# Kernel tuning notes

Measured on AMD Instinct MI355X. Metric: run time of the kernel, lower is better.

## Reference

```python
import jax, jax.numpy as jnp
import numpy as np
from jax import lax

EPS = 1e-6

def _instance_norm(x):
    # torch: std over flattened spatial, unbiased (ddof=1), + 1e-6
    b, c = x.shape[:2]
    xf = x.reshape(b, c, -1)
    mean = xf.mean(axis=2)[:, :, None, None]
    std = (jnp.std(xf, axis=2, ddof=1) + EPS)[:, :, None, None]
    return (x - mean) / std

def _conv1x1(x, w, b):
    # w: [O, I], x: [B, I, H, W]
    return jnp.einsum('oi,bihw->bohw', w, x) + b[None, :, None, None]

def _adaattn(content, style, ckey, skey, fw, fb, gw, gb, hw, hb):
    F = _conv1x1(ckey, fw, fb)   # [b, Ck, hc, wc]
    G = _conv1x1(skey, gw, gb)   # [b, Ck, hs, ws]
    H = _conv1x1(style, hw, hb)  # [b, Cv, hs, ws]
    b_, Ck, hc, wc = F.shape
    hs, ws = G.shape[2], G.shape[3]
    Fq = F.reshape(b_, Ck, hc * wc).transpose(0, 2, 1)   # [b, Nc, Ck]
    Gk = G.reshape(b_, Ck, hs * ws)                      # [b, Ck, Ns]
    Vs = H.reshape(b_, -1, hs * ws).transpose(0, 2, 1)   # [b, Ns, Cv]
    # Ns == hs*ws <= max_sample (4096) for these shapes -> no subsampling branch
    S = jax.nn.softmax(jnp.einsum('bnc,bcm->bnm', Fq, Gk), axis=-1)  # [b, Nc, Ns]
    mean = jnp.einsum('bnm,bmv->bnv', S, Vs)              # attention-weighted mean
    ex2 = jnp.einsum('bnm,bmv->bnv', S, Vs * Vs)          # E[x^2]
    std = jnp.sqrt(jax.nn.relu(ex2 - mean * mean))        # sqrt(relu(E[x^2]-E[x]^2))
    mean = mean.reshape(b_, hc, wc, -1).transpose(0, 3, 1, 2)
    std = std.reshape(b_, hc, wc, -1).transpose(0, 3, 1, 2)
    return std * _instance_norm(content) + mean

def _upsample2(x):
    return jnp.repeat(jnp.repeat(x, 2, axis=2), 2, axis=3)

def _conv3x3_reflect(x, w, b):
    xp = jnp.pad(x, ((0, 0), (0, 0), (1, 1), (1, 1)), mode='reflect')
    y = lax.conv_general_dilated(xp, w, window_strides=(1, 1), padding='VALID',
                                 dimension_numbers=('NCHW', 'OIHW', 'NCHW'))
    return y + b[None, :, None, None]


def setup_inputs() -> dict:
    key = jax.random.key(0)
    ks = jax.random.split(key, 16)
    f32 = jnp.float32
    d = {}
    d['content4_1'] = jax.random.normal(ks[0], (1, 512, 128, 128), f32)
    d['style4_1'] = jax.random.normal(ks[1], (1, 512, 64, 64), f32)
    d['content5_1'] = jax.random.normal(ks[2], (1, 512, 64, 64), f32)
    d['style5_1'] = jax.random.normal(ks[3], (1, 512, 32, 32), f32)
    d['content4_1_key'] = jax.random.normal(ks[4], (1, 960, 128, 128), f32)
    d['style4_1_key'] = jax.random.normal(ks[5], (1, 960, 64, 64), f32)
    d['content5_1_key'] = jax.random.normal(ks[6], (1, 1472, 64, 64), f32)
    d['style5_1_key'] = jax.random.normal(ks[7], (1, 1472, 32, 32), f32)
    def w2(k, o, i):
        return jax.random.normal(k, (o, i), f32) / np.sqrt(i).astype(np.float32)
    d['f4_w'] = w2(ks[8], 960, 960); d['f4_b'] = jnp.zeros((960,), f32)
    d['g4_w'] = w2(ks[9], 960, 960); d['g4_b'] = jnp.zeros((960,), f32)
    d['h4_w'] = w2(ks[10], 512, 512); d['h4_b'] = jnp.zeros((512,), f32)
    d['f5_w'] = w2(ks[11], 1472, 1472); d['f5_b'] = jnp.zeros((1472,), f32)
    d['g5_w'] = w2(ks[12], 1472, 1472); d['g5_b'] = jnp.zeros((1472,), f32)
    d['h5_w'] = w2(ks[13], 512, 512); d['h5_b'] = jnp.zeros((512,), f32)
    d['conv_w'] = jax.random.normal(ks[14], (512, 512, 3, 3), f32) / np.sqrt(512 * 9).astype(np.float32)
    d['conv_b'] = jnp.zeros((512,), f32)
    return d


def reference(content4_1, style4_1, content5_1, style5_1,
              content4_1_key, style4_1_key, content5_1_key, style5_1_key,
              f4_w, f4_b, g4_w, g4_b, h4_w, h4_b,
              f5_w, f5_b, g5_w, g5_b, h5_w, h5_b,
              conv_w, conv_b):
    a4 = _adaattn(content4_1, style4_1, content4_1_key, style4_1_key,
                  f4_w, f4_b, g4_w, g4_b, h4_w, h4_b)
    a5 = _adaattn(content5_1, style5_1, content5_1_key, style5_1_key,
                  f5_w, f5_b, g5_w, g5_b, h5_w, h5_b)
    return _conv3x3_reflect(a4 + _upsample2(a5), conv_w, conv_b)
```

## Files before the change

kernel.cpp:

```cpp
#include <hip/hip_runtime.h>
#include <math.h>


typedef _Float16 half8 __attribute__((ext_vector_type(8)));
typedef float f32x4 __attribute__((ext_vector_type(4)));

__device__ __forceinline__ void async16(const void* g, void* lds) {
    __builtin_amdgcn_global_load_lds(
        (const __attribute__((address_space(1))) void*)g,
        (__attribute__((address_space(3))) void*)lds, 16, 0, 0);
}

__device__ inline float wave_sum64(float v) {
#pragma unroll
    for (int o = 32; o > 0; o >>= 1) v += __shfl_xor(v, o, 64);
    return v;
}

template <int OUT>
__global__ __launch_bounds__(256, 2) void mgemm_hl(
    const _Float16* __restrict__ Ahi, const _Float16* __restrict__ Alo,
    const _Float16* __restrict__ Bhi, const _Float16* __restrict__ Blo,
    float* __restrict__ Cf, _Float16* __restrict__ Chi,
    _Float16* __restrict__ Clo, int K, int lda, int ldb, int ldc) {
    __shared__ _Float16 Ash[4096], Asl[4096], Bsh[4096], Bsl[4096];
    const int t = threadIdx.x, wave = t >> 6, lane = t & 63;
    const int bm = blockIdx.y * 128, bn = blockIdx.x * 128;
    const int wr = (wave >> 1) * 64, wc = (wave & 1) * 64;
    const int lq = lane >> 4, lr = lane & 15;
    const int srow = wave * 32 + (lane >> 2);
    const int scolg = (lane & 3) ^ ((lane >> 3) & 3);

    f32x4 acc[4][4] = {};

    const size_t aoff = (size_t)(bm + srow) * lda * 2 + scolg * 16;
    const size_t boff = (size_t)(bn + srow) * ldb * 2 + scolg * 16;
    const char* pAh = (const char*)Ahi + aoff;
    const char* pAl = (const char*)Alo + aoff;
    const char* pBh = (const char*)Bhi + boff;
    const char* pBl = (const char*)Blo + boff;
    const size_t ar = (size_t)16 * lda * 2, br = (size_t)16 * ldb * 2;
    _Float16* dAh = Ash + wave * 1024;
    _Float16* dAl = Asl + wave * 1024;
    _Float16* dBh = Bsh + wave * 1024;
    _Float16* dBl = Bsl + wave * 1024;
    const int key = (lr >> 1) & 3;

    for (int k0 = 0; k0 < K; k0 += 32) {
        __syncthreads();
        async16(pAh, dAh);
        async16(pAh + ar, dAh + 512);
        async16(pAl, dAl);
        async16(pAl + ar, dAl + 512);
        async16(pBh, dBh);
        async16(pBh + br, dBh + 512);
        async16(pBl, dBl);
        async16(pBl + br, dBl + 512);
        pAh += 64;
        pAl += 64;
        pBh += 64;
        pBl += 64;
        __syncthreads();

        half8 ah[4], al[4], bh[4], bl[4];
#pragma unroll
        for (int i = 0; i < 4; i++) {
            const int ro = (wr + i * 16 + lr) * 32 + ((lq ^ key) * 8);
            ah[i] = *(const half8*)&Ash[ro];
            al[i] = *(const half8*)&Asl[ro];
        }
#pragma unroll
        for (int j = 0; j < 4; j++) {
            const int ro = (wc + j * 16 + lr) * 32 + ((lq ^ key) * 8);
            bh[j] = *(const half8*)&Bsh[ro];
            bl[j] = *(const half8*)&Bsl[ro];
        }
#pragma unroll
        for (int i = 0; i < 4; i++)
#pragma unroll
            for (int j = 0; j < 4; j++) {
                acc[i][j] = __builtin_amdgcn_mfma_f32_16x16x32_f16(
                    ah[i], bl[j], acc[i][j], 0, 0, 0);
                acc[i][j] = __builtin_amdgcn_mfma_f32_16x16x32_f16(
                    al[i], bh[j], acc[i][j], 0, 0, 0);
                acc[i][j] = __builtin_amdgcn_mfma_f32_16x16x32_f16(
                    ah[i], bh[j], acc[i][j], 0, 0, 0);
            }
    }
#pragma unroll
    for (int i = 0; i < 4; i++) {
        const int m0 = bm + wr + i * 16 + lq * 4;
#pragma unroll
        for (int j = 0; j < 4; j++) {
            const int n = bn + wc + j * 16 + lr;
#pragma unroll
            for (int r = 0; r < 4; r++) {
                const float v = acc[i][j][r];
                const size_t o = (size_t)(m0 + r) * ldc + n;
                if (OUT == 0) {
                    Cf[o] = v;
                } else {
                    _Float16 h = (_Float16)v;
                    Chi[o] = h;
                    Clo[o] = (_Float16)(v - (float)h);
                }
            }
        }
    }
}

template <int BIAS_MODE, int OUT_MODE, bool CONV>
__global__ __launch_bounds__(256, 2) void mgemm16(
    const _Float16* __restrict__ A, const _Float16* __restrict__ B,
    const float* __restrict__ bias, float* __restrict__ Cf,
    _Float16* __restrict__ Ch, int K, int lda, int ldb, int ldc,
    size_t splitStride) {
    __shared__ _Float16 As[128 * 32];
    __shared__ _Float16 Bs[128 * 32];
    const int t = threadIdx.x, wave = t >> 6, lane = t & 63;
    const int bm = blockIdx.y * 128, bn = blockIdx.x * 128;
    const int kbase = blockIdx.z * K;
    const int wr = (wave >> 1) * 64, wc = (wave & 1) * 64;
    const int lq = lane >> 4, lr = lane & 15;
    const int srow = wave * 32 + (lane >> 2);
    const int scolg = (lane & 3) ^ ((lane >> 3) & 3);

    f32x4 acc[4][4] = {};

    const char* Ap = (const char*)A +
                     ((size_t)(bm + srow) * lda + kbase) * 2 + scolg * 16;
    const char* Bp = (const char*)B +
                     ((size_t)(bn + srow) * ldb + kbase) * 2 + scolg * 16;
    const size_t Astep = (size_t)16 * lda * 2;
    const size_t Bstep = (size_t)16 * ldb * 2;
    _Float16* As0 = &As[(wave * 32) * 32];
    _Float16* As1 = &As[(wave * 32 + 16) * 32];
    _Float16* Bs0 = &Bs[(wave * 32) * 32];
    _Float16* Bs1 = &Bs[(wave * 32 + 16) * 32];
    const int key = (lr >> 1) & 3;

    for (int k0 = 0; k0 < K; k0 += 32) {
        __syncthreads();
        async16(Ap, As0);
        async16(Ap + Astep, As1);
        if (CONV) {
            const int kg = kbase + k0;
            const int rI = kg >> 9;
            const int dy = rI / 3, dx = rI - 3 * dy;
            const int ci0 = kg & 511;
            const char* Bc =
                (const char*)B +
                (((size_t)(blockIdx.x + dy) * 130 + srow + dx) * 512 + ci0) * 2 +
                scolg * 16;
            async16(Bc, Bs0);
            async16(Bc + (size_t)16 * 512 * 2, Bs1);
        } else {
            async16(Bp, Bs0);
            async16(Bp + Bstep, Bs1);
            Bp += 64;
        }
        Ap += 64;
        __syncthreads();

        half8 af[4], bf[4];
#pragma unroll
        for (int i = 0; i < 4; i++)
            af[i] = *(const half8*)&As[(wr + i * 16 + lr) * 32 + (lq ^ key) * 8];
#pragma unroll
        for (int j = 0; j < 4; j++)
            bf[j] = *(const half8*)&Bs[(wc + j * 16 + lr) * 32 + (lq ^ key) * 8];
#pragma unroll
        for (int i = 0; i < 4; i++)
#pragma unroll
            for (int j = 0; j < 4; j++)
                acc[i][j] = __builtin_amdgcn_mfma_f32_16x16x32_f16(
                    af[i], bf[j], acc[i][j], 0, 0, 0);
    }

    float* Co = (OUT_MODE == 0) ? Cf + (size_t)blockIdx.z * splitStride : nullptr;
#pragma unroll
    for (int i = 0; i < 4; i++) {
        const int m0 = bm + wr + i * 16 + lq * 4;
#pragma unroll
        for (int j = 0; j < 4; j++) {
            const int n = bn + wc + j * 16 + lr;
#pragma unroll
            for (int r = 0; r < 4; r++) {
                const int m = m0 + r;
                float v = acc[i][j][r];
                if (BIAS_MODE == 2) v += bias[m];
                if (OUT_MODE == 0) {
                    Co[(size_t)m * ldc + n] = v;
                } else {
                    Ch[(size_t)m * ldc + n] = (_Float16)v;
                    Ch[(size_t)(m + 512) * ldc + n] = (_Float16)(v * v);
                }
            }
        }
    }
}

__global__ __launch_bounds__(256) void transpose_hilo(
    const float* __restrict__ src, _Float16* __restrict__ dsthi,
    _Float16* __restrict__ dstlo, long srcld, int dstld, int nvalid,
    int cvalid) {
    __shared__ float tile[32][33];
    const int t = threadIdx.x, tx = t & 31, ty = t >> 5;
    const int n0 = blockIdx.x * 32, c0 = blockIdx.y * 32;
    const int n = n0 + tx;
#pragma unroll
    for (int i = 0; i < 4; i++) {
        int c = c0 + ty + i * 8;
        tile[ty + i * 8][tx] =
            (c < cvalid && n < nvalid) ? src[(size_t)c * srcld + n] : 0.f;
    }
    __syncthreads();
#pragma unroll
    for (int i = 0; i < 4; i++) {
        int nn = ty + i * 8;
        float v = tile[tx][nn];
        _Float16 h = (_Float16)v;
        size_t o = (size_t)(n0 + nn) * dstld + c0 + tx;
        dsthi[o] = h;
        dstlo[o] = (_Float16)(v - (float)h);
    }
}

__global__ __launch_bounds__(256) void transpose_cvt16(
    const float* __restrict__ src, _Float16* __restrict__ dst, long srcld,
    int dstld) {
    __shared__ float tile[32][33];
    const int t = threadIdx.x, tx = t & 31, ty = t >> 5;
    const int n0 = blockIdx.x * 32, c0 = blockIdx.y * 32;
#pragma unroll
    for (int i = 0; i < 4; i++)
        tile[ty + i * 8][tx] = src[(size_t)(c0 + ty + i * 8) * srcld + n0 + tx];
    __syncthreads();
#pragma unroll
    for (int i = 0; i < 4; i++) {
        int nn = ty + i * 8;
        dst[(size_t)(n0 + nn) * dstld + c0 + tx] = (_Float16)tile[tx][nn];
    }
}

__global__ __launch_bounds__(256) void cvt16(const float* __restrict__ src,
                                             _Float16* __restrict__ dst) {
    int i = blockIdx.x * 256 + threadIdx.x;
    dst[i] = (_Float16)src[i];
}

__global__ __launch_bounds__(256) void convw_perm(const float* __restrict__ src,
                                                  _Float16* __restrict__ dst) {
    int idx = blockIdx.x * 256 + threadIdx.x;
    int o = idx / 4608, rem = idx - o * 4608;
    int r = rem >> 9, ci = rem & 511;
    dst[idx] = (_Float16)src[(size_t)o * 4608 + ci * 9 + r];
}

__global__ __launch_bounds__(256) void fold_vec(
    const float* __restrict__ mat, const float* __restrict__ vec,
    const float* __restrict__ addc, float* __restrict__ outv, int C, int Nout,
    long ldm) {
    __shared__ float red[4][64];
    const int t = threadIdx.x, lane = t & 63, seg = t >> 6;
    const int n = blockIdx.x * 64 + lane;
    const int chunk = (C + 3) >> 2;
    const int start = seg * chunk;
    const int end = min(C, start + chunk);
    float s0 = 0.f, s1 = 0.f, s2 = 0.f, s3 = 0.f;
    if (n < Nout) {
        int c = start;
        for (; c + 3 < end; c += 4) {
            s0 = fmaf(vec[c], mat[(size_t)c * ldm + n], s0);
            s1 = fmaf(vec[c + 1], mat[(size_t)(c + 1) * ldm + n], s1);
            s2 = fmaf(vec[c + 2], mat[(size_t)(c + 2) * ldm + n], s2);
            s3 = fmaf(vec[c + 3], mat[(size_t)(c + 3) * ldm + n], s3);
        }
        for (; c < end; c++) s0 = fmaf(vec[c], mat[(size_t)c * ldm + n], s0);
    }
    red[seg][lane] = (s0 + s1) + (s2 + s3);
    __syncthreads();
    if (seg == 0 && n < Nout)
        outv[n] = red[0][lane] + red[1][lane] + red[2][lane] + red[3][lane] +
                  (addc ? addc[0] : 0.f);
}

__global__ __launch_bounds__(256) void dotbb(const float* __restrict__ a,
                                             const float* __restrict__ b,
                                             float* __restrict__ out, int C) {
    __shared__ float red[4];
    const int t = threadIdx.x;
    float s = 0.f;
    for (int c = t; c < C; c += 256) s = fmaf(a[c], b[c], s);
    s = wave_sum64(s);
    if ((t & 63) == 0) red[t >> 6] = s;
    __syncthreads();
    if (t == 0) out[0] = red[0] + red[1] + red[2] + red[3];
}

__global__ __launch_bounds__(256) void softmax_f16(
    const float* __restrict__ L, const float* __restrict__ rr,
    _Float16* __restrict__ S, int cols) {
    __shared__ float red_m[4], red_s[4];
    const int t = threadIdx.x;
    const float* p = L + (size_t)blockIdx.x * cols;
    _Float16* q = S + (size_t)blockIdx.x * cols;
    float mt = -3.0e38f, st = 0.f;
    for (int c = t; c < cols; c += 256) {
        float v = p[c] + rr[c];
        if (v > mt) {
            st = st * __expf(mt - v) + 1.f;
            mt = v;
        } else {
            st += __expf(v - mt);
        }
    }
#pragma unroll
    for (int o = 32; o > 0; o >>= 1) {
        float m2 = __shfl_xor(mt, o, 64), s2 = __shfl_xor(st, o, 64);
        float m = fmaxf(mt, m2);
        st = st * __expf(mt - m) + s2 * __expf(m2 - m);
        mt = m;
    }
    if ((t & 63) == 0) {
        red_m[t >> 6] = mt;
        red_s[t >> 6] = st;
    }
    __syncthreads();
    float M = fmaxf(fmaxf(red_m[0], red_m[1]), fmaxf(red_m[2], red_m[3]));
    float Ssum = red_s[0] * __expf(red_m[0] - M) +
                 red_s[1] * __expf(red_m[1] - M) +
                 red_s[2] * __expf(red_m[2] - M) +
                 red_s[3] * __expf(red_m[3] - M);
    float inv = 1.f / Ssum;
    for (int c = t; c < cols; c += 256)
        q[c] = (_Float16)(__expf(p[c] + rr[c] - M) * inv);
}

__global__ __launch_bounds__(256) void chanstats_kernel(
    const float* __restrict__ x, float* __restrict__ cm,
    float* __restrict__ cstd, int N) {
    __shared__ float rs[4], rs2[4];
    const int t = threadIdx.x;
    const float* p = x + (size_t)blockIdx.x * N;
    float s = 0.f, s2 = 0.f;
    for (int i = t; i < N; i += 256) {
        float v = p[i];
        s += v;
        s2 = fmaf(v, v, s2);
    }
    s = wave_sum64(s);
    s2 = wave_sum64(s2);
    if ((t & 63) == 0) {
        rs[t >> 6] = s;
        rs2[t >> 6] = s2;
    }
    __syncthreads();
    if (t == 0) {
        float S = rs[0] + rs[1] + rs[2] + rs[3];
        float S2 = rs2[0] + rs2[1] + rs2[2] + rs2[3];
        float mean = S / N;
        float var = fmaxf((S2 - S * mean) / (N - 1), 0.f);
        cm[blockIdx.x] = mean;
        cstd[blockIdx.x] = sqrtf(var) + 1e-6f;
    }
}

__global__ __launch_bounds__(256) void epilogue5(
    const float* __restrict__ pv, const float* __restrict__ content,
    const float* __restrict__ cm, const float* __restrict__ cstd,
    _Float16* __restrict__ a5t) {
    int idx = blockIdx.x * 256 + threadIdx.x;
    int n = idx >> 9, c = idx & 511;
    float mean = pv[(size_t)n * 1024 + c];
    float ex2 = pv[(size_t)n * 1024 + 512 + c];
    float sd = sqrtf(fmaxf(ex2 - mean * mean, 0.f));
    float cn = (content[(size_t)c * 4096 + n] - cm[c]) / cstd[c];
    a5t[idx] = (_Float16)(fmaf(sd, cn, mean));
}

__global__ __launch_bounds__(256) void epilogue4(
    const float* __restrict__ part, const float* __restrict__ content,
    const float* __restrict__ cm, const float* __restrict__ cstd,
    const _Float16* __restrict__ a5t, _Float16* __restrict__ pad4t, int n0) {
    int idx = blockIdx.x * 256 + threadIdx.x;
    int r = idx >> 9, c = idx & 511;
    int n = n0 + r;
    const size_t SS = (size_t)1024 * 1024;
    float mean = 0.f, ex2 = 0.f;
#pragma unroll
    for (int z = 0; z < 4; z++) {
        mean += part[z * SS + (size_t)r * 1024 + c];
        ex2 += part[z * SS + (size_t)r * 1024 + 512 + c];
    }
    float sd = sqrtf(fmaxf(ex2 - mean * mean, 0.f));
    float cn = (content[(size_t)c * 16384 + n] - cm[c]) / cstd[c];
    int y = n >> 7, x = n & 127;
    float up = (float)a5t[(size_t)((y >> 1) * 64 + (x >> 1)) * 512 + c];
    pad4t[(size_t)((y + 1) * 130 + (x + 1)) * 512 + c] =
        (_Float16)(fmaf(sd, cn, mean) + up);
}

__global__ __launch_bounds__(256) void border_kernel(_Float16* __restrict__ pad) {
    int idx = blockIdx.x * 256 + threadIdx.x;
    int pos = idx >> 9, c = idx & 511;
    int py, px;
    if (pos < 130) { py = 0; px = pos; }
    else if (pos < 260) { py = 129; px = pos - 130; }
    else if (pos < 388) { py = pos - 260 + 1; px = 0; }
    else { py = pos - 388 + 1; px = 129; }
    int sy = py == 0 ? 2 : (py == 129 ? 127 : py);
    int sx = px == 0 ? 2 : (px == 129 ? 127 : px);
    pad[(size_t)(py * 130 + px) * 512 + c] =
        pad[(size_t)(sy * 130 + sx) * 512 + c];
}


extern "C" void kernel_launch(void* const* d_in, const int* in_sizes, int n_in,
                              void* d_out, int out_size, void* d_ws,
                              size_t ws_size, hipStream_t stream) {
    (void)in_sizes; (void)n_in; (void)out_size; (void)ws_size;
    const float* content4 = (const float*)d_in[0];
    const float* style4 = (const float*)d_in[1];
    const float* content5 = (const float*)d_in[2];
    const float* style5 = (const float*)d_in[3];
    const float* ckey4 = (const float*)d_in[4];
    const float* skey4 = (const float*)d_in[5];
    const float* ckey5 = (const float*)d_in[6];
    const float* skey5 = (const float*)d_in[7];
    const float* f4w = (const float*)d_in[8];
    const float* f4b = (const float*)d_in[9];
    const float* g4w = (const float*)d_in[10];
    const float* g4b = (const float*)d_in[11];
    const float* h4w = (const float*)d_in[12];
    const float* h4b = (const float*)d_in[13];
    const float* f5w = (const float*)d_in[14];
    const float* f5b = (const float*)d_in[15];
    const float* g5w = (const float*)d_in[16];
    const float* g5b = (const float*)d_in[17];
    const float* h5w = (const float*)d_in[18];
    const float* h5b = (const float*)d_in[19];
    const float* convw = (const float*)d_in[20];
    const float* convb = (const float*)d_in[21];
    float* out = (float*)d_out;
    char* ws = (char*)d_ws;

    _Float16* PAD4T = (_Float16*)(ws + 0);
    _Float16* A5T = (_Float16*)(ws + 17305600);
    float* STATS = (float*)(ws + 21499904);
    _Float16* H4W = (_Float16*)(ws + 21508096);
    _Float16* H5W = (_Float16*)(ws + 22032384);
    _Float16* CONVW = (_Float16*)(ws + 22556672);
    float* U5 = (float*)(ws + 27275264);
    float* R5 = (float*)(ws + 27283456);
    float* U4 = (float*)(ws + 27291648);
    float* R4 = (float*)(ws + 27299840);
    float* BB5 = (float*)(ws + 27316224);
    float* BB4 = (float*)(ws + 27316480);
    char* A0 = ws + 27320320;

    float* cm4 = STATS, *cstd4 = STATS + 512, *cm5 = STATS + 1024,
         *cstd5 = STATS + 1536;

    chanstats_kernel<<<512, 256, 0, stream>>>(content5, cm5, cstd5, 4096);
    chanstats_kernel<<<512, 256, 0, stream>>>(content4, cm4, cstd4, 16384);
    cvt16<<<1024, 256, 0, stream>>>(h4w, H4W);
    cvt16<<<1024, 256, 0, stream>>>(h5w, H5W);
    convw_perm<<<9216, 256, 0, stream>>>(convw, CONVW);

    {
        _Float16* M5h = (_Float16*)(A0 + 0);
        _Float16* M5l = (_Float16*)(A0 + 4718592);
        _Float16* FWh = (_Float16*)(A0 + 9437184);
        _Float16* FWl = (_Float16*)(A0 + 14155776);
        _Float16* GWh = (_Float16*)(A0 + 18874368);
        _Float16* GWl = (_Float16*)(A0 + 23592960);
        _Float16* SKh = (_Float16*)(A0 + 9437184);
        _Float16* SKl = (_Float16*)(A0 + 12582912);
        _Float16* T5h = (_Float16*)(A0 + 15728640);
        _Float16* T5l = (_Float16*)(A0 + 18874368);
        _Float16* STT5 = (_Float16*)(A0 + 0);
        _Float16* HCAT5 = (_Float16*)(A0 + 1048576);
        _Float16* CKh = (_Float16*)(A0 + 22020096);
        _Float16* CKl = (_Float16*)(A0 + 34603008);
        float* LOG5 = (float*)(A0 + 47185920);
        _Float16* S5 = (_Float16*)(A0 + 63963136);

        dotbb<<<1, 256, 0, stream>>>(f5b, g5b, BB5, 1472);
        fold_vec<<<23, 256, 0, stream>>>(g5w, f5b, nullptr, U5, 1472, 1472, 1472);
        fold_vec<<<16, 256, 0, stream>>>(skey5, U5, BB5, R5, 1472, 1024, 1024);

        transpose_hilo<<<dim3(48, 48), 256, 0, stream>>>(f5w, FWh, FWl, 1472,
                                                         1536, 1472, 1472);
        transpose_hilo<<<dim3(48, 48), 256, 0, stream>>>(g5w, GWh, GWl, 1472,
                                                         1536, 1472, 1472);
        mgemm_hl<1><<<dim3(12, 12), 256, 0, stream>>>(
            FWh, FWl, GWh, GWl, nullptr, M5h, M5l, 1536, 1536, 1536, 1536);
        transpose_hilo<<<dim3(32, 48), 256, 0, stream>>>(skey5, SKh, SKl, 1024,
                                                         1536, 1024, 1472);
        mgemm_hl<1><<<dim3(12, 8), 256, 0, stream>>>(
            SKh, SKl, M5h, M5l, nullptr, T5h, T5l, 1536, 1536, 1536, 1536);
        transpose_cvt16<<<dim3(32, 16), 256, 0, stream>>>(style5, STT5, 1024, 512);
        mgemm16<2, 2, false><<<dim3(8, 4), 256, 0, stream>>>(
            H5W, STT5, h5b, nullptr, HCAT5, 512, 512, 512, 1024, 0);
        transpose_hilo<<<dim3(128, 48), 256, 0, stream>>>(ckey5, CKh, CKl, 4096,
                                                          1536, 4096, 1472);
        mgemm_hl<0><<<dim3(8, 32), 256, 0, stream>>>(
            CKh, CKl, T5h, T5l, LOG5, nullptr, nullptr, 1536, 1536, 1536, 1024);
        softmax_f16<<<4096, 256, 0, stream>>>(LOG5, R5, S5, 1024);
        mgemm16<0, 0, false><<<dim3(8, 32), 256, 0, stream>>>(
            S5, HCAT5, nullptr, LOG5 , nullptr, 1024, 1024, 1024, 1024,
            (size_t)4096 * 1024);
        epilogue5<<<8192, 256, 0, stream>>>(LOG5, content5, cm5, cstd5, A5T);
    }

    {
        _Float16* T4h = (_Float16*)(A0 + 0);
        _Float16* T4l = (_Float16*)(A0 + 8388608);
        _Float16* M4h = (_Float16*)(A0 + 16777216);
        _Float16* M4l = (_Float16*)(A0 + 18874368);
        _Float16* FWh = (_Float16*)(A0 + 20971520);
        _Float16* FWl = (_Float16*)(A0 + 23068672);
        _Float16* GWh = (_Float16*)(A0 + 25165824);
        _Float16* GWl = (_Float16*)(A0 + 27262976);
        _Float16* SKh = (_Float16*)(A0 + 29360128);
        _Float16* SKl = (_Float16*)(A0 + 37748736);
        _Float16* STT4 = (_Float16*)(A0 + 16777216);
        _Float16* HCAT4 = (_Float16*)(A0 + 20971520);
        _Float16* CKh = (_Float16*)(A0 + 29360128);
        _Float16* CKl = (_Float16*)(A0 + 31457280);
        _Float16* S4 = (_Float16*)(A0 + 33554432);
        float* LOGR = (float*)(A0 + 41943040);

        dotbb<<<1, 256, 0, stream>>>(f4b, g4b, BB4, 960);
        fold_vec<<<15, 256, 0, stream>>>(g4w, f4b, nullptr, U4, 960, 960, 960);
        fold_vec<<<64, 256, 0, stream>>>(skey4, U4, BB4, R4, 960, 4096, 4096);

        transpose_hilo<<<dim3(32, 32), 256, 0, stream>>>(f4w, FWh, FWl, 960,
                                                         1024, 960, 960);
        transpose_hilo<<<dim3(32, 32), 256, 0, stream>>>(g4w, GWh, GWl, 960,
                                                         1024, 960, 960);
        mgemm_hl<1><<<dim3(8, 8), 256, 0, stream>>>(
            FWh, FWl, GWh, GWl, nullptr, M4h, M4l, 1024, 1024, 1024, 1024);
        transpose_hilo<<<dim3(128, 32), 256, 0, stream>>>(skey4, SKh, SKl, 4096,
                                                          1024, 4096, 960);
        mgemm_hl<1><<<dim3(8, 32), 256, 0, stream>>>(
            SKh, SKl, M4h, M4l, nullptr, T4h, T4l, 1024, 1024, 1024, 1024);
        transpose_cvt16<<<dim3(128, 16), 256, 0, stream>>>(style4, STT4, 4096, 512);
        mgemm16<2, 2, false><<<dim3(32, 4), 256, 0, stream>>>(
            H4W, STT4, h4b, nullptr, HCAT4, 512, 512, 512, 4096, 0);

        for (int chunk = 0; chunk < 16; chunk++) {
            const int n0 = chunk * 1024;
            transpose_hilo<<<dim3(32, 32), 256, 0, stream>>>(
                ckey4 + n0, CKh, CKl, 16384, 1024, 1024, 960);
            mgemm_hl<0><<<dim3(32, 8), 256, 0, stream>>>(
                CKh, CKl, T4h, T4l, LOGR, nullptr, nullptr, 1024, 1024, 1024,
                4096);
            softmax_f16<<<1024, 256, 0, stream>>>(LOGR, R4, S4, 4096);
            mgemm16<0, 0, false><<<dim3(8, 8, 4), 256, 0, stream>>>(
                S4, HCAT4, nullptr, LOGR , nullptr, 1024, 4096, 4096,
                1024, (size_t)1024 * 1024);
            epilogue4<<<2048, 256, 0, stream>>>(LOGR, content4, cm4, cstd4, A5T,
                                                PAD4T, n0);
        }
    }

    border_kernel<<<1032, 256, 0, stream>>>(PAD4T);
    mgemm16<2, 0, true><<<dim3(128, 4), 256, 0, stream>>>(
        CONVW, PAD4T, convb, out, nullptr, 4608, 4608, 512, 16384, 0);
}
```

Baseline: 2.429 ms.

## Double-buffer LDS tiles in GEMM kernels to overlap loads with MFMA

Both GEMM kernels (the hi/lo split-precision one and the plain fp16/conv one) now keep two LDS buffers. The global-to-LDS async copy for the next K tile is issued right after the barrier, so it runs while the MFMAs work on the current tile. This cuts the barriers per iteration from two to one and hides global load latency. In exchange, LDS use per block doubles (64KB for the hi/lo kernel), which may limit occupancy.

```diff
diff --git a/kernel.cpp b/kernel.cpp
--- a/kernel.cpp
+++ b/kernel.cpp
@@ -23,7 +23,7 @@
     const _Float16* __restrict__ Bhi, const _Float16* __restrict__ Blo,
     float* __restrict__ Cf, _Float16* __restrict__ Chi,
     _Float16* __restrict__ Clo, int K, int lda, int ldb, int ldc) {
-    __shared__ _Float16 Ash[4096], Asl[4096], Bsh[4096], Bsl[4096];
+    __shared__ _Float16 Ash[2][4096], Asl[2][4096], Bsh[2][4096], Bsl[2][4096];
     const int t = threadIdx.x, wave = t >> 6, lane = t & 63;
     const int bm = blockIdx.y * 128, bn = blockIdx.x * 128;
     const int wr = (wave >> 1) * 64, wc = (wave & 1) * 64;
@@ -40,40 +40,43 @@
     const char* pBh = (const char*)Bhi + boff;
     const char* pBl = (const char*)Blo + boff;
     const size_t ar = (size_t)16 * lda * 2, br = (size_t)16 * ldb * 2;
-    _Float16* dAh = Ash + wave * 1024;
-    _Float16* dAl = Asl + wave * 1024;
-    _Float16* dBh = Bsh + wave * 1024;
-    _Float16* dBl = Bsl + wave * 1024;
+    const int dst = wave * 1024;
     const int key = (lr >> 1) & 3;
 
-    for (int k0 = 0; k0 < K; k0 += 32) {
-        __syncthreads();
-        async16(pAh, dAh);
-        async16(pAh + ar, dAh + 512);
-        async16(pAl, dAl);
-        async16(pAl + ar, dAl + 512);
-        async16(pBh, dBh);
-        async16(pBh + br, dBh + 512);
-        async16(pBl, dBl);
-        async16(pBl + br, dBl + 512);
+    auto stage = [&](int buf) {
+        async16(pAh, &Ash[buf][dst]);
+        async16(pAh + ar, &Ash[buf][dst + 512]);
+        async16(pAl, &Asl[buf][dst]);
+        async16(pAl + ar, &Asl[buf][dst + 512]);
+        async16(pBh, &Bsh[buf][dst]);
+        async16(pBh + br, &Bsh[buf][dst + 512]);
+        async16(pBl, &Bsl[buf][dst]);
+        async16(pBl + br, &Bsl[buf][dst + 512]);
         pAh += 64;
         pAl += 64;
         pBh += 64;
         pBl += 64;
+    };
+
+    const int NT = K >> 5;
+    stage(0);
+    for (int tt = 0; tt < NT; tt++) {
         __syncthreads();
+        if (tt + 1 < NT) stage((tt + 1) & 1);
+        const int cb = tt & 1;
 
         half8 ah[4], al[4], bh[4], bl[4];
 #pragma unroll
         for (int i = 0; i < 4; i++) {
             const int ro = (wr + i * 16 + lr) * 32 + ((lq ^ key) * 8);
-            ah[i] = *(const half8*)&Ash[ro];
-            al[i] = *(const half8*)&Asl[ro];
+            ah[i] = *(const half8*)&Ash[cb][ro];
+            al[i] = *(const half8*)&Asl[cb][ro];
         }
 #pragma unroll
         for (int j = 0; j < 4; j++) {
             const int ro = (wc + j * 16 + lr) * 32 + ((lq ^ key) * 8);
-            bh[j] = *(const half8*)&Bsh[ro];
-            bl[j] = *(const half8*)&Bsl[ro];
+            bh[j] = *(const half8*)&Bsh[cb][ro];
+            bl[j] = *(const half8*)&Bsl[cb][ro];
         }
 #pragma unroll
         for (int i = 0; i < 4; i++)
@@ -115,8 +118,8 @@
     const float* __restrict__ bias, float* __restrict__ Cf,
     _Float16* __restrict__ Ch, int K, int lda, int ldb, int ldc,
     size_t splitStride) {
-    __shared__ _Float16 As[128 * 32];
-    __shared__ _Float16 Bs[128 * 32];
+    __shared__ _Float16 As[2][4096];
+    __shared__ _Float16 Bs[2][4096];
     const int t = threadIdx.x, wave = t >> 6, lane = t & 63;
     const int bm = blockIdx.y * 128, bn = blockIdx.x * 128;
     const int kbase = blockIdx.z * K;
@@ -133,16 +136,13 @@
                      ((size_t)(bn + srow) * ldb + kbase) * 2 + scolg * 16;
     const size_t Astep = (size_t)16 * lda * 2;
     const size_t Bstep = (size_t)16 * ldb * 2;
-    _Float16* As0 = &As[(wave * 32) * 32];
-    _Float16* As1 = &As[(wave * 32 + 16) * 32];
-    _Float16* Bs0 = &Bs[(wave * 32) * 32];
-    _Float16* Bs1 = &Bs[(wave * 32 + 16) * 32];
+    const int dst = wave * 1024;
     const int key = (lr >> 1) & 3;
 
-    for (int k0 = 0; k0 < K; k0 += 32) {
-        __syncthreads();
-        async16(Ap, As0);
-        async16(Ap + Astep, As1);
+    auto stage = [&](int buf, int k0) {
+        async16(Ap, &As[buf][dst]);
+        async16(Ap + Astep, &As[buf][dst + 512]);
+        Ap += 64;
         if (CONV) {
             const int kg = kbase + k0;
             const int rI = kg >> 9;
@@ -152,23 +152,31 @@
                 (const char*)B +
                 (((size_t)(blockIdx.x + dy) * 130 + srow + dx) * 512 + ci0) * 2 +
                 scolg * 16;
-            async16(Bc, Bs0);
-            async16(Bc + (size_t)16 * 512 * 2, Bs1);
+            async16(Bc, &Bs[buf][dst]);
+            async16(Bc + (size_t)16 * 512 * 2, &Bs[buf][dst + 512]);
         } else {
-            async16(Bp, Bs0);
-            async16(Bp + Bstep, Bs1);
+            async16(Bp, &Bs[buf][dst]);
+            async16(Bp + Bstep, &Bs[buf][dst + 512]);
             Bp += 64;
         }
-        Ap += 64;
+    };
+
+    const int NT = K >> 5;
+    stage(0, 0);
+    for (int tt = 0; tt < NT; tt++) {
         __syncthreads();
+        if (tt + 1 < NT) stage((tt + 1) & 1, (tt + 1) << 5);
+        const int cb = tt & 1;
 
         half8 af[4], bf[4];
 #pragma unroll
         for (int i = 0; i < 4; i++)
-            af[i] = *(const half8*)&As[(wr + i * 16 + lr) * 32 + (lq ^ key) * 8];
+            af[i] =
+                *(const half8*)&As[cb][(wr + i * 16 + lr) * 32 + (lq ^ key) * 8];
 #pragma unroll
         for (int j = 0; j < 4; j++)
-            bf[j] = *(const half8*)&Bs[(wc + j * 16 + lr) * 32 + (lq ^ key) * 8];
+            bf[j] =
+                *(const half8*)&Bs[cb][(wc + j * 16 + lr) * 32 + (lq ^ key) * 8];
 #pragma unroll
         for (int i = 0; i < 4; i++)
 #pragma unroll
```

New measurement: 2.413 ms. No clear change (-0.7%).

## Split-K the hi/lo GEMMs and fuse partial sums into a vectorized softmax

Applied to the files above, without the earlier changes.

Adds a blockIdx.z split-K dimension to the hi/lo compensated GEMM, which now writes fp32 partials. A new combine kernel sums the partials and re-splits them into hi/lo halves, and the logits partials are summed inside a new register-resident, vectorized softmax. The PV GEMMs also get a larger split-K, and the epilogues sum more partials. The aim is to raise occupancy on small launch grids (64-256 blocks) across the many CUs, at the cost of extra partial buffers, extra memory traffic and reshuffled scratch offsets.

```diff
diff --git a/kernel.cpp b/kernel.cpp
--- a/kernel.cpp
+++ b/kernel.cpp
@@ -3,6 +3,7 @@
 
 
 typedef _Float16 half8 __attribute__((ext_vector_type(8)));
+typedef _Float16 half4 __attribute__((ext_vector_type(4)));
 typedef float f32x4 __attribute__((ext_vector_type(4)));
 
 __device__ __forceinline__ void async16(const void* g, void* lds) {
@@ -17,15 +18,15 @@
     return v;
 }
 
-template <int OUT>
 __global__ __launch_bounds__(256, 2) void mgemm_hl(
     const _Float16* __restrict__ Ahi, const _Float16* __restrict__ Alo,
     const _Float16* __restrict__ Bhi, const _Float16* __restrict__ Blo,
-    float* __restrict__ Cf, _Float16* __restrict__ Chi,
-    _Float16* __restrict__ Clo, int K, int lda, int ldb, int ldc) {
+    float* __restrict__ Cf, int K, int lda, int ldb, int ldc,
+    size_t splitStride) {
     __shared__ _Float16 Ash[4096], Asl[4096], Bsh[4096], Bsl[4096];
     const int t = threadIdx.x, wave = t >> 6, lane = t & 63;
     const int bm = blockIdx.y * 128, bn = blockIdx.x * 128;
+    const int kbase = blockIdx.z * K;
     const int wr = (wave >> 1) * 64, wc = (wave & 1) * 64;
     const int lq = lane >> 4, lr = lane & 15;
     const int srow = wave * 32 + (lane >> 2);
@@ -33,8 +34,8 @@
 
     f32x4 acc[4][4] = {};
 
-    const size_t aoff = (size_t)(bm + srow) * lda * 2 + scolg * 16;
-    const size_t boff = (size_t)(bn + srow) * ldb * 2 + scolg * 16;
+    const size_t aoff = ((size_t)(bm + srow) * lda + kbase) * 2 + scolg * 16;
+    const size_t boff = ((size_t)(bn + srow) * ldb + kbase) * 2 + scolg * 16;
     const char* pAh = (const char*)Ahi + aoff;
     const char* pAl = (const char*)Alo + aoff;
     const char* pBh = (const char*)Bhi + boff;
@@ -87,6 +88,7 @@
                     ah[i], bh[j], acc[i][j], 0, 0, 0);
             }
     }
+    float* Co = Cf + (size_t)blockIdx.z * splitStride;
 #pragma unroll
     for (int i = 0; i < 4; i++) {
         const int m0 = bm + wr + i * 16 + lq * 4;
@@ -94,17 +96,8 @@
         for (int j = 0; j < 4; j++) {
             const int n = bn + wc + j * 16 + lr;
 #pragma unroll
-            for (int r = 0; r < 4; r++) {
-                const float v = acc[i][j][r];
-                const size_t o = (size_t)(m0 + r) * ldc + n;
-                if (OUT == 0) {
-                    Cf[o] = v;
-                } else {
-                    _Float16 h = (_Float16)v;
-                    Chi[o] = h;
-                    Clo[o] = (_Float16)(v - (float)h);
-                }
-            }
+            for (int r = 0; r < 4; r++)
+                Co[(size_t)(m0 + r) * ldc + n] = acc[i][j][r];
         }
     }
 }
@@ -200,6 +193,17 @@
     }
 }
 
+__global__ __launch_bounds__(256) void combine_hilo(
+    const float* __restrict__ part, _Float16* __restrict__ hi,
+    _Float16* __restrict__ lo, int nz, size_t zs) {
+    size_t i = (size_t)blockIdx.x * 256 + threadIdx.x;
+    float s = 0.f;
+    for (int z = 0; z < nz; z++) s += part[z * zs + i];
+    _Float16 h = (_Float16)s;
+    hi[i] = h;
+    lo[i] = (_Float16)(s - (float)h);
+}
+
 __global__ __launch_bounds__(256) void transpose_hilo(
     const float* __restrict__ src, _Float16* __restrict__ dsthi,
     _Float16* __restrict__ dstlo, long srcld, int dstld, int nvalid,
@@ -298,43 +302,55 @@
     if (t == 0) out[0] = red[0] + red[1] + red[2] + red[3];
 }
 
-__global__ __launch_bounds__(256) void softmax_f16(
-    const float* __restrict__ L, const float* __restrict__ rr,
-    _Float16* __restrict__ S, int cols) {
-    __shared__ float red_m[4], red_s[4];
+template <int NPER, int NZ>
+__global__ __launch_bounds__(256) void softmax2(const float* __restrict__ L,
+                                                const float* __restrict__ rr,
+                                                _Float16* __restrict__ S,
+                                                size_t zs) {
+    constexpr int NV = NPER / 4;
+    __shared__ float redm[4], reds[4];
     const int t = threadIdx.x;
-    const float* p = L + (size_t)blockIdx.x * cols;
-    _Float16* q = S + (size_t)blockIdx.x * cols;
-    float mt = -3.0e38f, st = 0.f;
-    for (int c = t; c < cols; c += 256) {
-        float v = p[c] + rr[c];
-        if (v > mt) {
-            st = st * __expf(mt - v) + 1.f;
-            mt = v;
-        } else {
-            st += __expf(v - mt);
-        }
-    }
-#pragma unroll
-    for (int o = 32; o > 0; o >>= 1) {
-        float m2 = __shfl_xor(mt, o, 64), s2 = __shfl_xor(st, o, 64);
-        float m = fmaxf(mt, m2);
-        st = st * __expf(mt - m) + s2 * __expf(m2 - m);
-        mt = m;
-    }
-    if ((t & 63) == 0) {
-        red_m[t >> 6] = mt;
-        red_s[t >> 6] = st;
-    }
+    const float* p = L + (size_t)blockIdx.x * (NPER * 256);
+    _Float16* q = S + (size_t)blockIdx.x * (NPER * 256);
+    f32x4 v[NV];
+    float m = -3.0e38f;
+#pragma unroll
+    for (int i = 0; i < NV; i++) {
+        const int c = t * 4 + i * 1024;
+        f32x4 x = *(const f32x4*)(p + c);
+        if (NZ == 2) x = x + *(const f32x4*)(p + zs + c);
+        x = x + *(const f32x4*)(rr + c);
+        v[i] = x;
+        m = fmaxf(m, fmaxf(fmaxf(x[0], x[1]), fmaxf(x[2], x[3])));
+    }
+#pragma unroll
+    for (int o = 32; o > 0; o >>= 1) m = fmaxf(m, __shfl_xor(m, o, 64));
+    if ((t & 63) == 0) redm[t >> 6] = m;
     __syncthreads();
-    float M = fmaxf(fmaxf(red_m[0], red_m[1]), fmaxf(red_m[2], red_m[3]));
-    float Ssum = red_s[0] * __expf(red_m[0] - M) +
-                 red_s[1] * __expf(red_m[1] - M) +
-                 red_s[2] * __expf(red_m[2] - M) +
-                 red_s[3] * __expf(red_m[3] - M);
-    float inv = 1.f / Ssum;
-    for (int c = t; c < cols; c += 256)
-        q[c] = (_Float16)(__expf(p[c] + rr[c] - M) * inv);
+    m = fmaxf(fmaxf(redm[0], redm[1]), fmaxf(redm[2], redm[3]));
+    float s = 0.f;
+#pragma unroll
+    for (int i = 0; i < NV; i++) {
+        f32x4 x = v[i];
+#pragma unroll
+        for (int j = 0; j < 4; j++) {
+            x[j] = __expf(x[j] - m);
+            s += x[j];
+        }
+        v[i] = x;
+    }
+    s = wave_sum64(s);
+    if ((t & 63) == 0) reds[t >> 6] = s;
+    __syncthreads();
+    const float inv = 1.f / (reds[0] + reds[1] + reds[2] + reds[3]);
+#pragma unroll
+    for (int i = 0; i < NV; i++) {
+        const int c = t * 4 + i * 1024;
+        half4 h;
+#pragma unroll
+        for (int j = 0; j < 4; j++) h[j] = (_Float16)(v[i][j] * inv);
+        *(half4*)(q + c) = h;
+    }
 }
 
 __global__ __launch_bounds__(256) void chanstats_kernel(
@@ -372,8 +388,10 @@
     _Float16* __restrict__ a5t) {
     int idx = blockIdx.x * 256 + threadIdx.x;
     int n = idx >> 9, c = idx & 511;
-    float mean = pv[(size_t)n * 1024 + c];
-    float ex2 = pv[(size_t)n * 1024 + 512 + c];
+    const size_t SS = (size_t)4096 * 1024;
+    float mean = pv[(size_t)n * 1024 + c] + pv[SS + (size_t)n * 1024 + c];
+    float ex2 =
+        pv[(size_t)n * 1024 + 512 + c] + pv[SS + (size_t)n * 1024 + 512 + c];
     float sd = sqrtf(fmaxf(ex2 - mean * mean, 0.f));
     float cn = (content[(size_t)c * 4096 + n] - cm[c]) / cstd[c];
     a5t[idx] = (_Float16)(fmaf(sd, cn, mean));
@@ -389,7 +407,7 @@
     const size_t SS = (size_t)1024 * 1024;
     float mean = 0.f, ex2 = 0.f;
 #pragma unroll
-    for (int z = 0; z < 4; z++) {
+    for (int z = 0; z < 8; z++) {
         mean += part[z * SS + (size_t)r * 1024 + c];
         ex2 += part[z * SS + (size_t)r * 1024 + 512 + c];
     }
@@ -469,22 +487,24 @@
     convw_perm<<<9216, 256, 0, stream>>>(convw, CONVW);
 
     {
-        _Float16* M5h = (_Float16*)(A0 + 0);
-        _Float16* M5l = (_Float16*)(A0 + 4718592);
+        _Float16* STT5 = (_Float16*)(A0 + 0);
+        _Float16* HCAT5 = (_Float16*)(A0 + 1048576);
+        _Float16* T5h = (_Float16*)(A0 + 3145728);
+        _Float16* T5l = (_Float16*)(A0 + 6291456);
         _Float16* FWh = (_Float16*)(A0 + 9437184);
         _Float16* FWl = (_Float16*)(A0 + 14155776);
         _Float16* GWh = (_Float16*)(A0 + 18874368);
         _Float16* GWl = (_Float16*)(A0 + 23592960);
+        float* PM5 = (float*)(A0 + 28311552);
+        _Float16* M5h = (_Float16*)(A0 + 56623104);
+        _Float16* M5l = (_Float16*)(A0 + 61341696);
         _Float16* SKh = (_Float16*)(A0 + 9437184);
         _Float16* SKl = (_Float16*)(A0 + 12582912);
-        _Float16* T5h = (_Float16*)(A0 + 15728640);
-        _Float16* T5l = (_Float16*)(A0 + 18874368);
-        _Float16* STT5 = (_Float16*)(A0 + 0);
-        _Float16* HCAT5 = (_Float16*)(A0 + 1048576);
-        _Float16* CKh = (_Float16*)(A0 + 22020096);
-        _Float16* CKl = (_Float16*)(A0 + 34603008);
-        float* LOG5 = (float*)(A0 + 47185920);
-        _Float16* S5 = (_Float16*)(A0 + 63963136);
+        float* PT5 = (float*)(A0 + 15728640);
+        _Float16* CKh = (_Float16*)(A0 + 9437184);
+        _Float16* CKl = (_Float16*)(A0 + 22020096);
+        float* LOG5 = (float*)(A0 + 34603008);
+        _Float16* S5 = (_Float16*)(A0 + 9437184);
 
         dotbb<<<1, 256, 0, stream>>>(f5b, g5b, BB5, 1472);
         fold_vec<<<23, 256, 0, stream>>>(g5w, f5b, nullptr, U5, 1472, 1472, 1472);
@@ -494,22 +514,30 @@
                                                          1536, 1472, 1472);
         transpose_hilo<<<dim3(48, 48), 256, 0, stream>>>(g5w, GWh, GWl, 1472,
                                                          1536, 1472, 1472);
-        mgemm_hl<1><<<dim3(12, 12), 256, 0, stream>>>(
-            FWh, FWl, GWh, GWl, nullptr, M5h, M5l, 1536, 1536, 1536, 1536);
+        mgemm_hl<<<dim3(12, 12, 3), 256, 0, stream>>>(
+            FWh, FWl, GWh, GWl, PM5, 512, 1536, 1536, 1536,
+            (size_t)1536 * 1536);
+        combine_hilo<<<9216, 256, 0, stream>>>(PM5, M5h, M5l, 3,
+                                               (size_t)1536 * 1536);
         transpose_hilo<<<dim3(32, 48), 256, 0, stream>>>(skey5, SKh, SKl, 1024,
                                                          1536, 1024, 1472);
-        mgemm_hl<1><<<dim3(12, 8), 256, 0, stream>>>(
-            SKh, SKl, M5h, M5l, nullptr, T5h, T5l, 1536, 1536, 1536, 1536);
+        mgemm_hl<<<dim3(12, 8, 3), 256, 0, stream>>>(
+            SKh, SKl, M5h, M5l, PT5, 512, 1536, 1536, 1536,
+            (size_t)1024 * 1536);
+        combine_hilo<<<6144, 256, 0, stream>>>(PT5, T5h, T5l, 3,
+                                               (size_t)1024 * 1536);
         transpose_cvt16<<<dim3(32, 16), 256, 0, stream>>>(style5, STT5, 1024, 512);
         mgemm16<2, 2, false><<<dim3(8, 4), 256, 0, stream>>>(
             H5W, STT5, h5b, nullptr, HCAT5, 512, 512, 512, 1024, 0);
         transpose_hilo<<<dim3(128, 48), 256, 0, stream>>>(ckey5, CKh, CKl, 4096,
                                                           1536, 4096, 1472);
-        mgemm_hl<0><<<dim3(8, 32), 256, 0, stream>>>(
-            CKh, CKl, T5h, T5l, LOG5, nullptr, nullptr, 1536, 1536, 1536, 1024);
-        softmax_f16<<<4096, 256, 0, stream>>>(LOG5, R5, S5, 1024);
-        mgemm16<0, 0, false><<<dim3(8, 32), 256, 0, stream>>>(
-            S5, HCAT5, nullptr, LOG5 , nullptr, 1024, 1024, 1024, 1024,
+        mgemm_hl<<<dim3(8, 32, 2), 256, 0, stream>>>(
+            CKh, CKl, T5h, T5l, LOG5, 768, 1536, 1536, 1024,
+            (size_t)4096 * 1024);
+        softmax2<4, 2><<<4096, 256, 0, stream>>>(LOG5, R5, S5,
+                                                 (size_t)4096 * 1024);
+        mgemm16<0, 0, false><<<dim3(8, 32, 2), 256, 0, stream>>>(
+            S5, HCAT5, nullptr, LOG5, nullptr, 512, 1024, 1024, 1024,
             (size_t)4096 * 1024);
         epilogue5<<<8192, 256, 0, stream>>>(LOG5, content5, cm5, cstd5, A5T);
     }
@@ -523,14 +551,16 @@
         _Float16* FWl = (_Float16*)(A0 + 23068672);
         _Float16* GWh = (_Float16*)(A0 + 25165824);
         _Float16* GWl = (_Float16*)(A0 + 27262976);
-        _Float16* SKh = (_Float16*)(A0 + 29360128);
-        _Float16* SKl = (_Float16*)(A0 + 37748736);
-        _Float16* STT4 = (_Float16*)(A0 + 16777216);
-        _Float16* HCAT4 = (_Float16*)(A0 + 20971520);
+        float* PM4 = (float*)(A0 + 29360128);
+        _Float16* SKh = (_Float16*)(A0 + 20971520);
+        _Float16* SKl = (_Float16*)(A0 + 29360128);
+        float* PT4 = (float*)(A0 + 37748736);
+        _Float16* HCAT4 = (_Float16*)(A0 + 16777216);
+        _Float16* STT4 = (_Float16*)(A0 + 25165824);
         _Float16* CKh = (_Float16*)(A0 + 29360128);
         _Float16* CKl = (_Float16*)(A0 + 31457280);
-        _Float16* S4 = (_Float16*)(A0 + 33554432);
-        float* LOGR = (float*)(A0 + 41943040);
+        _Float16* S4 = (_Float16*)(A0 + 25165824);
+        float* LOGR = (float*)(A0 + 33554432);
 
         dotbb<<<1, 256, 0, stream>>>(f4b, g4b, BB4, 960);
         fold_vec<<<15, 256, 0, stream>>>(g4w, f4b, nullptr, U4, 960, 960, 960);
@@ -540,12 +570,18 @@
                                                          1024, 960, 960);
         transpose_hilo<<<dim3(32, 32), 256, 0, stream>>>(g4w, GWh, GWl, 960,
                                                          1024, 960, 960);
-        mgemm_hl<1><<<dim3(8, 8), 256, 0, stream>>>(
-            FWh, FWl, GWh, GWl, nullptr, M4h, M4l, 1024, 1024, 1024, 1024);
+        mgemm_hl<<<dim3(8, 8, 4), 256, 0, stream>>>(
+            FWh, FWl, GWh, GWl, PM4, 256, 1024, 1024, 1024,
+            (size_t)1024 * 1024);
+        combine_hilo<<<4096, 256, 0, stream>>>(PM4, M4h, M4l, 4,
+                                               (size_t)1024 * 1024);
         transpose_hilo<<<dim3(128, 32), 256, 0, stream>>>(skey4, SKh, SKl, 4096,
                                                           1024, 4096, 960);
-        mgemm_hl<1><<<dim3(8, 32), 256, 0, stream>>>(
-            SKh, SKl, M4h, M4l, nullptr, T4h, T4l, 1024, 1024, 1024, 1024);
+        mgemm_hl<<<dim3(8, 32, 2), 256, 0, stream>>>(
+            SKh, SKl, M4h, M4l, PT4, 512, 1024, 1024, 1024,
+            (size_t)4096 * 1024);
+        combine_hilo<<<16384, 256, 0, stream>>>(PT4, T4h, T4l, 2,
+                                                (size_t)4096 * 1024);
         transpose_cvt16<<<dim3(128, 16), 256, 0, stream>>>(style4, STT4, 4096, 512);
         mgemm16<2, 2, false><<<dim3(32, 4), 256, 0, stream>>>(
             H4W, STT4, h4b, nullptr, HCAT4, 512, 512, 512, 4096, 0);
@@ -554,13 +590,14 @@
             const int n0 = chunk * 1024;
             transpose_hilo<<<dim3(32, 32), 256, 0, stream>>>(
                 ckey4 + n0, CKh, CKl, 16384, 1024, 1024, 960);
-            mgemm_hl<0><<<dim3(32, 8), 256, 0, stream>>>(
-                CKh, CKl, T4h, T4l, LOGR, nullptr, nullptr, 1024, 1024, 1024,
-                4096);
-            softmax_f16<<<1024, 256, 0, stream>>>(LOGR, R4, S4, 4096);
-            mgemm16<0, 0, false><<<dim3(8, 8, 4), 256, 0, stream>>>(
-                S4, HCAT4, nullptr, LOGR , nullptr, 1024, 4096, 4096,
-                1024, (size_t)1024 * 1024);
+            mgemm_hl<<<dim3(32, 8, 2), 256, 0, stream>>>(
+                CKh, CKl, T4h, T4l, LOGR, 512, 1024, 1024, 4096,
+                (size_t)1024 * 4096);
+            softmax2<16, 2><<<1024, 256, 0, stream>>>(LOGR, R4, S4,
+                                                      (size_t)1024 * 4096);
+            mgemm16<0, 0, false><<<dim3(8, 8, 8), 256, 0, stream>>>(
+                S4, HCAT4, nullptr, LOGR, nullptr, 512, 4096, 4096, 1024,
+                (size_t)1024 * 1024);
             epilogue4<<<2048, 256, 0, stream>>>(LOGR, content4, cm4, cstd4, A5T,
                                                 PAD4T, n0);
         }
```

Result: faster. 1.993 ms (-17.9%).
